# Optimization experiments

Hardware: AMD Instinct MI355X
Metric: run time of the kernel (lower is better)

Reference implementation:

```python
import jax, jax.numpy as jnp
import numpy as np

H, W = 160, 480
C_IMG = 256
VFC = [64, 128, 256]
N_PTS = 120000


def setup_inputs() -> dict:
    key = jax.random.key(0)
    ks = jax.random.split(key, 16)
    inp = {}
    inp["img_feat"] = jax.random.normal(ks[0], (C_IMG, H, W), jnp.float32)
    inp["seg_prob"] = jax.random.uniform(ks[1], (1, 2, H, W), jnp.float32)
    for i, c in enumerate(VFC):
        inp[f"voxel_feat{i}"] = jax.random.normal(ks[2 + i], (N_PTS, c), jnp.float32)
        x = jax.random.randint(ks[5 + i], (N_PTS,), 0, W + 1)  # col coord in [0, W]
        y = jax.random.randint(ks[8 + i], (N_PTS,), 0, H + 1)  # row coord in [0, H]
        inp[f"img_grid{i}"] = jnp.stack([x, y], axis=1).astype(jnp.int32)
    inp["red_w0"] = jax.random.normal(ks[11], (VFC[2], VFC[0]), jnp.float32) * 0.05
    inp["red_b0"] = jnp.zeros((VFC[2],), jnp.float32)
    inp["red_w1"] = jax.random.normal(ks[12], (VFC[2], VFC[1]), jnp.float32) * 0.05
    inp["red_b1"] = jnp.zeros((VFC[2],), jnp.float32)
    inp["sb_w"] = jax.random.normal(ks[13], (1, C_IMG + VFC[2], 3, 3), jnp.float32) * 0.02
    inp["sb_b"] = jnp.zeros((1,), jnp.float32)
    return inp


def pts2img(coor, pts_feat):
    # coor: [N,2] int (x, y); torch does coor[:, [1,0]] then grid[y, x] = feat
    c = pts_feat.shape[1]
    grid = jnp.zeros((H + 1, W + 1, c), pts_feat.dtype)
    grid = grid.at[coor[:, 1], coor[:, 0]].set(pts_feat, mode="drop")
    return grid[:-1, :-1].transpose(2, 0, 1)  # [C, H, W]


def reference(img_feat, seg_prob, voxel_feat0, voxel_feat1, voxel_feat2,
              img_grid0, img_grid1, img_grid2,
              red_w0, red_b0, red_w1, red_b1, sb_w, sb_b):
    # seg-gated image features
    enhanced = img_feat * seg_prob[0, 1][None]  # [C_IMG, H, W]

    # level 0: scatter + 1x1 conv (64 -> 256)
    p0 = pts2img(img_grid0, voxel_feat0)
    p0 = jnp.einsum('chw,oc->ohw', p0, red_w0) + red_b0[:, None, None]
    # level 1: scatter + 1x1 conv (128 -> 256)
    p1 = pts2img(img_grid1, voxel_feat1)
    p1 = jnp.einsum('chw,oc->ohw', p1, red_w1) + red_b1[:, None, None]
    # level 2: scatter only (already 256)
    p2 = pts2img(img_grid2, voxel_feat2)
    pt_img = p0 + p1 + p2  # [256, H, W]

    fused = jnp.concatenate([enhanced, pt_img], axis=0)[None]  # [1, 512, H, W]
    conv = jax.lax.conv_general_dilated(
        fused, sb_w, window_strides=(1, 1), padding='SAME',
        dimension_numbers=('NCHW', 'OIHW', 'NCHW'))
    conv = conv + sb_b[None, :, None, None]
    attention_map = jax.nn.sigmoid(conv[0])  # [1, H, W]
    return enhanced * attention_map
```

## Files before the change

### kernel.cpp

```cpp
#include <hip/hip_runtime.h>
#include <math.h>

#define H 160
#define W 480
#define HW 76800
#define CIMG 256
#define NPTS 120000
#define T9S 12


__global__ __launch_bounds__(256) void scatter_winners(
    const int2* __restrict__ g0, const int2* __restrict__ g1, const int2* __restrict__ g2,
    int* __restrict__ w0, int* __restrict__ w1, int* __restrict__ w2) {
  int j = blockIdx.x * blockDim.x + threadIdx.x;
  if (j >= NPTS) return;
  int2 c;
  c = g0[j];
  if ((unsigned)c.x < W && (unsigned)c.y < H) atomicMax(&w0[c.y * W + c.x], j);
  c = g1[j];
  if ((unsigned)c.x < W && (unsigned)c.y < H) atomicMax(&w1[c.y * W + c.x], j);
  c = g2[j];
  if ((unsigned)c.x < W && (unsigned)c.y < H) atomicMax(&w2[c.y * W + c.x], j);
}

__global__ __launch_bounds__(256) void prep_weights(
    const float* __restrict__ rw0, const float* __restrict__ rw1,
    const float* __restrict__ rb0, const float* __restrict__ rb1,
    const float* __restrict__ sbw,
    float* __restrict__ Weff0, float* __restrict__ Weff1, float* __restrict__ bconst) {
  int t = blockIdx.x * blockDim.x + threadIdx.x;
  if (t < 576) {
    int jj = t / 64, k = t % 64;
    float s = 0.f;
    for (int c = 0; c < 256; ++c) s = fmaf(rw0[c * 64 + k], sbw[(256 + c) * 9 + jj], s);
    Weff0[jj * 64 + k] = s;
  } else if (t < 1728) {
    int tt = t - 576;
    int jj = tt / 128, k = tt % 128;
    float s = 0.f;
    for (int c = 0; c < 256; ++c) s = fmaf(rw1[c * 128 + k], sbw[(256 + c) * 9 + jj], s);
    Weff1[jj * 128 + k] = s;
  } else if (t < 1737) {
    int jj = t - 1728;
    float s = 0.f;
    for (int c = 0; c < 256; ++c) s = fmaf(rb0[c] + rb1[c], sbw[(256 + c) * 9 + jj], s);
    bconst[jj] = s;
  }
}

__global__ __launch_bounds__(256) void t_img_kernel(
    const float* __restrict__ img, const float* __restrict__ seg,
    const float* __restrict__ sbw, float* __restrict__ t9) {
  int p = blockIdx.x * blockDim.x + threadIdx.x;
  float acc[9];
#pragma unroll
  for (int j = 0; j < 9; ++j) acc[j] = 0.f;
#pragma unroll 8
  for (int c = 0; c < 256; ++c) {
    float v = img[c * HW + p];
    const float* wr = sbw + c * 9;
#pragma unroll
    for (int j = 0; j < 9; ++j) acc[j] = fmaf(v, wr[j], acc[j]);
  }
  float s = seg[HW + p];
  float4 o0 = make_float4(acc[0] * s, acc[1] * s, acc[2] * s, acc[3] * s);
  float4 o1 = make_float4(acc[4] * s, acc[5] * s, acc[6] * s, acc[7] * s);
  float4 o2 = make_float4(acc[8] * s, 0.f, 0.f, 0.f);
  float* dst = t9 + (size_t)p * T9S;
  *(float4*)(dst + 0) = o0;
  *(float4*)(dst + 4) = o1;
  *(float4*)(dst + 8) = o2;
}

#define PIXW 8
__global__ __launch_bounds__(256) void t_vox_kernel(
    const float* __restrict__ vf0, const float* __restrict__ vf1, const float* __restrict__ vf2,
    const int* __restrict__ w0m, const int* __restrict__ w1m, const int* __restrict__ w2m,
    const float* __restrict__ Weff0, const float* __restrict__ Weff1,
    const float* __restrict__ sbw, float* __restrict__ t9) {
  int lane = threadIdx.x & 63;
  int waveId = (blockIdx.x * blockDim.x + threadIdx.x) >> 6;

  float wg0[9], wg1[2][9], wg2[4][9];
#pragma unroll
  for (int j = 0; j < 9; ++j) wg0[j] = Weff0[j * 64 + lane];
#pragma unroll
  for (int j = 0; j < 9; ++j) {
    wg1[0][j] = Weff1[j * 128 + 2 * lane + 0];
    wg1[1][j] = Weff1[j * 128 + 2 * lane + 1];
  }
#pragma unroll
  for (int i = 0; i < 4; ++i)
#pragma unroll
    for (int j = 0; j < 9; ++j) wg2[i][j] = sbw[(256 + 4 * lane + i) * 9 + j];

  int pix0 = waveId * PIXW;
  for (int q = 0; q < PIXW; ++q) {
    int pix = pix0 + q;
    int w0 = w0m[pix], w1 = w1m[pix], w2 = w2m[pix];
    float acc[9];
#pragma unroll
    for (int j = 0; j < 9; ++j) acc[j] = 0.f;
    if (w0 >= 0) {
      float v = vf0[(size_t)w0 * 64 + lane];
#pragma unroll
      for (int j = 0; j < 9; ++j) acc[j] = fmaf(v, wg0[j], acc[j]);
    }
    if (w1 >= 0) {
      float2 v = *(const float2*)(vf1 + (size_t)w1 * 128 + 2 * lane);
#pragma unroll
      for (int j = 0; j < 9; ++j) {
        acc[j] = fmaf(v.x, wg1[0][j], acc[j]);
        acc[j] = fmaf(v.y, wg1[1][j], acc[j]);
      }
    }
    if (w2 >= 0) {
      float4 v = *(const float4*)(vf2 + (size_t)w2 * 256 + 4 * lane);
#pragma unroll
      for (int j = 0; j < 9; ++j) {
        acc[j] = fmaf(v.x, wg2[0][j], acc[j]);
        acc[j] = fmaf(v.y, wg2[1][j], acc[j]);
        acc[j] = fmaf(v.z, wg2[2][j], acc[j]);
        acc[j] = fmaf(v.w, wg2[3][j], acc[j]);
      }
    }
#pragma unroll
    for (int j = 0; j < 9; ++j) {
      float v = acc[j];
      v += __shfl_xor(v, 1);
      v += __shfl_xor(v, 2);
      v += __shfl_xor(v, 4);
      v += __shfl_xor(v, 8);
      v += __shfl_xor(v, 16);
      v += __shfl_xor(v, 32);
      acc[j] = v;
    }
    if (lane < 9) {
      float v = acc[0];
#pragma unroll
      for (int j = 1; j < 9; ++j) v = (lane == j) ? acc[j] : v;
      t9[(size_t)pix * T9S + lane] += v;
    }
  }
}

__global__ __launch_bounds__(256) void conv_sig_kernel(
    const float* __restrict__ t9, const float* __restrict__ bconst,
    const float* __restrict__ sbb, const float* __restrict__ seg,
    float* __restrict__ sa) {
  int p = blockIdx.x * blockDim.x + threadIdx.x;
  int y = p / W, x = p - y * W;
  float s = sbb[0];
#pragma unroll
  for (int dy = -1; dy <= 1; ++dy) {
#pragma unroll
    for (int dx = -1; dx <= 1; ++dx) {
      int yy = y + dy, xx = x + dx;
      if ((unsigned)yy < H && (unsigned)xx < W) {
        int j = (dy + 1) * 3 + (dx + 1);
        s += t9[(size_t)(yy * W + xx) * T9S + j] + bconst[j];
      }
    }
  }
  float att = 1.f / (1.f + expf(-s));
  sa[p] = att * seg[HW + p];
}

__global__ __launch_bounds__(256) void final_mul_kernel(
    const float* __restrict__ img, const float* __restrict__ sa, float* __restrict__ out) {
  int i = blockIdx.x * blockDim.x + threadIdx.x;
  int e = i * 4;
  int p = e % HW;
  float4 v = *(const float4*)(img + e);
  float4 g = *(const float4*)(sa + p);
  float4 o = make_float4(v.x * g.x, v.y * g.y, v.z * g.z, v.w * g.w);
  *(float4*)(out + e) = o;
}

extern "C" void kernel_launch(void* const* d_in, const int* in_sizes, int n_in,
                              void* d_out, int out_size, void* d_ws, size_t ws_size,
                              hipStream_t stream) {
  const float* img = (const float*)d_in[0];
  const float* seg = (const float*)d_in[1];
  int iV0 = 2, iG0 = 3, iV1 = 4, iG1 = 5, iV2 = 6, iG2 = 7;
  if (in_sizes[3] != 2 * NPTS) {
    iV0 = 2; iV1 = 3; iV2 = 4; iG0 = 5; iG1 = 6; iG2 = 7;
  }
  const float* vf0 = (const float*)d_in[iV0];
  const float* vf1 = (const float*)d_in[iV1];
  const float* vf2 = (const float*)d_in[iV2];
  const int2* g0 = (const int2*)d_in[iG0];
  const int2* g1 = (const int2*)d_in[iG1];
  const int2* g2 = (const int2*)d_in[iG2];
  const float* rw0 = (const float*)d_in[8];
  const float* rb0 = (const float*)d_in[9];
  const float* rw1 = (const float*)d_in[10];
  const float* rb1 = (const float*)d_in[11];
  const float* sbw = (const float*)d_in[12];
  const float* sbb = (const float*)d_in[13];

  char* ws = (char*)d_ws;
  int* w0m = (int*)(ws + 0);
  int* w1m = (int*)(ws + 307200);
  int* w2m = (int*)(ws + 614400);
  float* t9 = (float*)(ws + 921600);
  float* Weff0 = (float*)(ws + 4608000);
  float* Weff1 = (float*)(ws + 4610304);
  float* bconst = (float*)(ws + 4614912);
  float* sa = (float*)(ws + 0);

  float* out = (float*)d_out;

  hipMemsetAsync(w0m, 0xFF, 3 * 307200, stream);
  prep_weights<<<7, 256, 0, stream>>>(rw0, rw1, rb0, rb1, sbw, Weff0, Weff1, bconst);
  scatter_winners<<<(NPTS + 255) / 256, 256, 0, stream>>>(g0, g1, g2, w0m, w1m, w2m);
  t_img_kernel<<<HW / 256, 256, 0, stream>>>(img, seg, sbw, t9);
  t_vox_kernel<<<HW / (4 * PIXW), 256, 0, stream>>>(vf0, vf1, vf2, w0m, w1m, w2m,
                                                    Weff0, Weff1, sbw, t9);
  conv_sig_kernel<<<HW / 256, 256, 0, stream>>>(t9, bconst, sbb, seg, sa);
  final_mul_kernel<<<(out_size / 4) / 256, 256, 0, stream>>>(img, sa, out);
}
```

Before: 414.8 us.

## Merge image and voxel tap kernels into one sliced grid with per-slice partials

Replaces the separate image-tap kernel and the wave-per-pixel voxel kernel with one kernel over a 2D grid of 5 slices. Two slices split the 256 image channels, one handles levels 0 and 1, and two split level 2's channels. Each thread handles one pixel and does a serial dot product over a feature row, so the wave shuffle reductions and the read-modify-write of t9 go away. The 9 taps from each slice are written to separate partial buffers that the conv kernel sums. This raises parallelism and removes a kernel launch, at the cost of a 5x larger t9 buffer, more reads in the conv kernel, and uncoalesced per-thread gathers of feature rows.

New measurement: 379.8 us. 1.09x faster.

```diff
diff --git a/kernel.cpp b/kernel.cpp
--- a/kernel.cpp
+++ b/kernel.cpp
@@ -4,10 +4,15 @@
 #define H 160
 #define W 480
 #define HW 76800
-#define CIMG 256
 #define NPTS 120000
-#define T9S 12
-
+#define NSLICE 5
+
+#define OFF_W1M 307200
+#define OFF_W2M 614400
+#define OFF_T9  921600
+#define OFF_WE0 19353600
+#define OFF_WE1 19356672
+#define OFF_BC  19362816
 
 __global__ __launch_bounds__(256) void scatter_winners(
     const int2* __restrict__ g0, const int2* __restrict__ g1, const int2* __restrict__ g2,
@@ -33,13 +38,13 @@
     int jj = t / 64, k = t % 64;
     float s = 0.f;
     for (int c = 0; c < 256; ++c) s = fmaf(rw0[c * 64 + k], sbw[(256 + c) * 9 + jj], s);
-    Weff0[jj * 64 + k] = s;
+    Weff0[k * 12 + jj] = s;
   } else if (t < 1728) {
     int tt = t - 576;
     int jj = tt / 128, k = tt % 128;
     float s = 0.f;
     for (int c = 0; c < 256; ++c) s = fmaf(rw1[c * 128 + k], sbw[(256 + c) * 9 + jj], s);
-    Weff1[jj * 128 + k] = s;
+    Weff1[k * 12 + jj] = s;
   } else if (t < 1737) {
     int jj = t - 1728;
     float s = 0.f;
@@ -48,100 +53,89 @@
   }
 }
 
-__global__ __launch_bounds__(256) void t_img_kernel(
+__global__ __launch_bounds__(256) void t9_kernel(
     const float* __restrict__ img, const float* __restrict__ seg,
+    const float* __restrict__ vf0, const float* __restrict__ vf1,
+    const float* __restrict__ vf2,
+    const int* __restrict__ w0m, const int* __restrict__ w1m, const int* __restrict__ w2m,
+    const float* __restrict__ We0, const float* __restrict__ We1,
     const float* __restrict__ sbw, float* __restrict__ t9) {
-  int p = blockIdx.x * blockDim.x + threadIdx.x;
+  int p = blockIdx.x * 256 + threadIdx.x;
+  int slice = blockIdx.y;
   float acc[9];
 #pragma unroll
   for (int j = 0; j < 9; ++j) acc[j] = 0.f;
-#pragma unroll 8
-  for (int c = 0; c < 256; ++c) {
-    float v = img[c * HW + p];
-    const float* wr = sbw + c * 9;
-#pragma unroll
-    for (int j = 0; j < 9; ++j) acc[j] = fmaf(v, wr[j], acc[j]);
-  }
-  float s = seg[HW + p];
-  float4 o0 = make_float4(acc[0] * s, acc[1] * s, acc[2] * s, acc[3] * s);
-  float4 o1 = make_float4(acc[4] * s, acc[5] * s, acc[6] * s, acc[7] * s);
-  float4 o2 = make_float4(acc[8] * s, 0.f, 0.f, 0.f);
-  float* dst = t9 + (size_t)p * T9S;
-  *(float4*)(dst + 0) = o0;
-  *(float4*)(dst + 4) = o1;
-  *(float4*)(dst + 8) = o2;
-}
-
-#define PIXW 8
-__global__ __launch_bounds__(256) void t_vox_kernel(
-    const float* __restrict__ vf0, const float* __restrict__ vf1, const float* __restrict__ vf2,
-    const int* __restrict__ w0m, const int* __restrict__ w1m, const int* __restrict__ w2m,
-    const float* __restrict__ Weff0, const float* __restrict__ Weff1,
-    const float* __restrict__ sbw, float* __restrict__ t9) {
-  int lane = threadIdx.x & 63;
-  int waveId = (blockIdx.x * blockDim.x + threadIdx.x) >> 6;
-
-  float wg0[9], wg1[2][9], wg2[4][9];
-#pragma unroll
-  for (int j = 0; j < 9; ++j) wg0[j] = Weff0[j * 64 + lane];
-#pragma unroll
-  for (int j = 0; j < 9; ++j) {
-    wg1[0][j] = Weff1[j * 128 + 2 * lane + 0];
-    wg1[1][j] = Weff1[j * 128 + 2 * lane + 1];
-  }
-#pragma unroll
-  for (int i = 0; i < 4; ++i)
-#pragma unroll
-    for (int j = 0; j < 9; ++j) wg2[i][j] = sbw[(256 + 4 * lane + i) * 9 + j];
-
-  int pix0 = waveId * PIXW;
-  for (int q = 0; q < PIXW; ++q) {
-    int pix = pix0 + q;
-    int w0 = w0m[pix], w1 = w1m[pix], w2 = w2m[pix];
-    float acc[9];
-#pragma unroll
-    for (int j = 0; j < 9; ++j) acc[j] = 0.f;
+
+  if (slice < 2) {
+    int c0 = slice * 128;
+#pragma unroll 8
+    for (int cc = 0; cc < 128; ++cc) {
+      int c = c0 + cc;
+      float v = img[c * HW + p];
+      const float* wr = sbw + c * 9;
+#pragma unroll
+      for (int j = 0; j < 9; ++j) acc[j] = fmaf(v, wr[j], acc[j]);
+    }
+    float s = seg[HW + p];
+#pragma unroll
+    for (int j = 0; j < 9; ++j) acc[j] *= s;
+  } else if (slice == 2) {
+    int w0 = w0m[p];
     if (w0 >= 0) {
-      float v = vf0[(size_t)w0 * 64 + lane];
-#pragma unroll
-      for (int j = 0; j < 9; ++j) acc[j] = fmaf(v, wg0[j], acc[j]);
-    }
+      const float4* r = (const float4*)(vf0 + (size_t)w0 * 64);
+#pragma unroll 8
+      for (int i = 0; i < 16; ++i) {
+        float4 v = r[i];
+        const float* wc = We0 + i * 48;
+#pragma unroll
+        for (int j = 0; j < 9; ++j) {
+          acc[j] = fmaf(v.x, wc[j], acc[j]);
+          acc[j] = fmaf(v.y, wc[12 + j], acc[j]);
+          acc[j] = fmaf(v.z, wc[24 + j], acc[j]);
+          acc[j] = fmaf(v.w, wc[36 + j], acc[j]);
+        }
+      }
+    }
+    int w1 = w1m[p];
     if (w1 >= 0) {
-      float2 v = *(const float2*)(vf1 + (size_t)w1 * 128 + 2 * lane);
-#pragma unroll
-      for (int j = 0; j < 9; ++j) {
-        acc[j] = fmaf(v.x, wg1[0][j], acc[j]);
-        acc[j] = fmaf(v.y, wg1[1][j], acc[j]);
-      }
-    }
+      const float4* r = (const float4*)(vf1 + (size_t)w1 * 128);
+#pragma unroll 8
+      for (int i = 0; i < 32; ++i) {
+        float4 v = r[i];
+        const float* wc = We1 + i * 48;
+#pragma unroll
+        for (int j = 0; j < 9; ++j) {
+          acc[j] = fmaf(v.x, wc[j], acc[j]);
+          acc[j] = fmaf(v.y, wc[12 + j], acc[j]);
+          acc[j] = fmaf(v.z, wc[24 + j], acc[j]);
+          acc[j] = fmaf(v.w, wc[36 + j], acc[j]);
+        }
+      }
+    }
+  } else {
+    int w2 = w2m[p];
     if (w2 >= 0) {
-      float4 v = *(const float4*)(vf2 + (size_t)w2 * 256 + 4 * lane);
-#pragma unroll
-      for (int j = 0; j < 9; ++j) {
-        acc[j] = fmaf(v.x, wg2[0][j], acc[j]);
-        acc[j] = fmaf(v.y, wg2[1][j], acc[j]);
-        acc[j] = fmaf(v.z, wg2[2][j], acc[j]);
-        acc[j] = fmaf(v.w, wg2[3][j], acc[j]);
-      }
-    }
-#pragma unroll
-    for (int j = 0; j < 9; ++j) {
-      float v = acc[j];
-      v += __shfl_xor(v, 1);
-      v += __shfl_xor(v, 2);
-      v += __shfl_xor(v, 4);
-      v += __shfl_xor(v, 8);
-      v += __shfl_xor(v, 16);
-      v += __shfl_xor(v, 32);
-      acc[j] = v;
-    }
-    if (lane < 9) {
-      float v = acc[0];
-#pragma unroll
-      for (int j = 1; j < 9; ++j) v = (lane == j) ? acc[j] : v;
-      t9[(size_t)pix * T9S + lane] += v;
-    }
-  }
+      int cbase = (slice - 3) * 128;
+      const float4* r = (const float4*)(vf2 + (size_t)w2 * 256 + cbase);
+#pragma unroll 8
+      for (int i = 0; i < 32; ++i) {
+        float4 v = r[i];
+        const float* wc = sbw + (256 + cbase + 4 * i) * 9;
+#pragma unroll
+        for (int j = 0; j < 9; ++j) {
+          acc[j] = fmaf(v.x, wc[j], acc[j]);
+          acc[j] = fmaf(v.y, wc[9 + j], acc[j]);
+          acc[j] = fmaf(v.z, wc[18 + j], acc[j]);
+          acc[j] = fmaf(v.w, wc[27 + j], acc[j]);
+        }
+      }
+    }
+  }
+
+  float* dst = t9 + ((size_t)slice * HW + p) * 12;
+  *(float4*)(dst + 0) = make_float4(acc[0], acc[1], acc[2], acc[3]);
+  *(float4*)(dst + 4) = make_float4(acc[4], acc[5], acc[6], acc[7]);
+  *(float4*)(dst + 8) = make_float4(acc[8], 0.f, 0.f, 0.f);
 }
 
 __global__ __launch_bounds__(256) void conv_sig_kernel(
@@ -158,7 +152,10 @@
       int yy = y + dy, xx = x + dx;
       if ((unsigned)yy < H && (unsigned)xx < W) {
         int j = (dy + 1) * 3 + (dx + 1);
-        s += t9[(size_t)(yy * W + xx) * T9S + j] + bconst[j];
+        size_t q = (size_t)(yy * W + xx) * 12 + j;
+        s += bconst[j];
+#pragma unroll
+        for (int b = 0; b < NSLICE; ++b) s += t9[(size_t)b * HW * 12 + q];
       }
     }
   }
@@ -201,12 +198,12 @@
 
   char* ws = (char*)d_ws;
   int* w0m = (int*)(ws + 0);
-  int* w1m = (int*)(ws + 307200);
-  int* w2m = (int*)(ws + 614400);
-  float* t9 = (float*)(ws + 921600);
-  float* Weff0 = (float*)(ws + 4608000);
-  float* Weff1 = (float*)(ws + 4610304);
-  float* bconst = (float*)(ws + 4614912);
+  int* w1m = (int*)(ws + OFF_W1M);
+  int* w2m = (int*)(ws + OFF_W2M);
+  float* t9 = (float*)(ws + OFF_T9);
+  float* Weff0 = (float*)(ws + OFF_WE0);
+  float* Weff1 = (float*)(ws + OFF_WE1);
+  float* bconst = (float*)(ws + OFF_BC);
   float* sa = (float*)(ws + 0);
 
   float* out = (float*)d_out;
@@ -214,9 +211,9 @@
   hipMemsetAsync(w0m, 0xFF, 3 * 307200, stream);
   prep_weights<<<7, 256, 0, stream>>>(rw0, rw1, rb0, rb1, sbw, Weff0, Weff1, bconst);
   scatter_winners<<<(NPTS + 255) / 256, 256, 0, stream>>>(g0, g1, g2, w0m, w1m, w2m);
-  t_img_kernel<<<HW / 256, 256, 0, stream>>>(img, seg, sbw, t9);
-  t_vox_kernel<<<HW / (4 * PIXW), 256, 0, stream>>>(vf0, vf1, vf2, w0m, w1m, w2m,
-                                                    Weff0, Weff1, sbw, t9);
+  dim3 tg(HW / 256, NSLICE);
+  t9_kernel<<<tg, 256, 0, stream>>>(img, seg, vf0, vf1, vf2, w0m, w1m, w2m,
+                                    Weff0, Weff1, sbw, t9);
   conv_sig_kernel<<<HW / 256, 256, 0, stream>>>(t9, bconst, sbb, seg, sa);
   final_mul_kernel<<<(out_size / 4) / 256, 256, 0, stream>>>(img, sa, out);
 }
```
